# Kernel tuning notes

Hardware: AMD Instinct MI355X
Metric: run time of the kernel (lower is better)

## Reference

```python
import jax, jax.numpy as jnp
import numpy as np

B, T, C = 2, 2048, 2048
H, HD = 16, 128          # n_head, head_dim
D_C, D_C1, D_ROPE = 512, 512, 64
D_NOPE = HD - D_ROPE     # 64
M = 4                    # move_slots
EPS = 1.1920929e-07      # torch fp32 rms_norm default eps


def _rope(x, cos, sin):
    # x: (B,T,h,D), cos/sin: (B,T,D//2) -> broadcast over head axis
    c = cos[:, :, None, :]
    s = sin[:, :, None, :]
    x1, x2 = jnp.split(x, 2, axis=-1)
    return jnp.concatenate([x1 * c + x2 * s, -x1 * s + x2 * c], axis=-1)


def _rmsnorm(x):
    return x * jax.lax.rsqrt(jnp.mean(x * x, axis=-1, keepdims=True) + EPS)


def setup_inputs() -> dict:
    key = jax.random.key(0)
    ks = jax.random.split(key, 8)
    # realistic decoupled-RoPE angles over d_rope//2 frequencies
    inv_freq = 1.0 / (10000.0 ** (np.arange(0, D_ROPE, 2) / D_ROPE))  # (32,)
    ang = np.arange(T)[:, None] * inv_freq[None, :]                   # (T,32)
    cos = jnp.broadcast_to(jnp.cos(ang)[None].astype(jnp.float32), (B, T, D_ROPE // 2))
    sin = jnp.broadcast_to(jnp.sin(ang)[None].astype(jnp.float32), (B, T, D_ROPE // 2))
    return {
        "x": jax.random.normal(ks[0], (B, T, C), jnp.float32),
        "ve": jax.random.normal(ks[1], (B, T, M * H * HD), jnp.float32),
        "cos": cos,
        "sin": sin,
        "w_down": jax.random.normal(ks[2], (C, D_C + D_C1 + D_ROPE), jnp.float32) * 0.02,
        "w_ukv": jax.random.normal(ks[3], (D_C, H * (D_NOPE + HD)), jnp.float32) * 0.02,
        "w_uq": jax.random.normal(ks[4], (D_C1, H * HD), jnp.float32) * 0.02,
        "w_gate": jax.random.normal(ks[5], (C, H * (M + 1)), jnp.float32) * 0.02,
        "w_proj": jax.random.normal(ks[6], (H * HD, C), jnp.float32) * 0.02,
        "window_size": 2048,
    }


def reference(x, ve, cos, sin, w_down, w_ukv, w_uq, w_gate, w_proj, window_size):
    # fused down projection, split into kv-latent / q-latent / rope part
    down = x @ w_down                                          # (B,T,1088)
    c_kv, c_q, k_rope_raw = jnp.split(down, [D_C, D_C + D_C1], axis=-1)

    kv = (c_kv @ w_ukv).reshape(B, T, H, D_NOPE + HD)
    k_nope, v = jnp.split(kv, [D_NOPE], axis=-1)               # (B,T,H,64), (B,T,H,128)

    k_rope = _rope(k_rope_raw.reshape(B, T, 1, D_ROPE), cos, sin)  # (B,T,1,64)

    # MoVE gating: per-head gate on v plus mixture over M value-embedding slots
    ve5 = ve.reshape(B, T, M, H, HD)
    gates = 2.0 * jax.nn.sigmoid(x @ w_gate).reshape(B, T, H, M + 1)
    v = gates[..., 0:1] * v + jnp.einsum('bthm,btmhd->bthd', gates[..., 1:], ve5)

    q = (c_q @ w_uq).reshape(B, T, H, HD)
    q_nope, q_rope = jnp.split(q, [D_NOPE], axis=-1)
    q_rope = _rope(q_rope, cos, sin)

    k = jnp.concatenate([k_nope, jnp.broadcast_to(k_rope, (B, T, H, D_ROPE))], axis=-1)
    q = jnp.concatenate([q_nope, q_rope], axis=-1)
    q, k = _rmsnorm(q), _rmsnorm(k)

    # sliding-window causal attention (flash_attn semantics: j<=i and i-j<=window)
    scale = 1.0 / float(np.sqrt(HD))
    scores = jnp.einsum('bthd,bshd->bhts', q, k) * scale       # (B,H,T,T)
    i = jnp.arange(T)[:, None]
    j = jnp.arange(T)[None, :]
    mask = (j <= i) & ((i - j) <= window_size)
    scores = jnp.where(mask, scores, -jnp.inf)
    attn = jax.nn.softmax(scores, axis=-1)
    y = jnp.einsum('bhts,bshd->bthd', attn, v)                 # (B,T,H,HD)

    return y.reshape(B, T, H * HD) @ w_proj                    # (B,T,C)
```

## Files before the change

### kernel.cpp

```cpp
#include <hip/hip_runtime.h>

typedef unsigned short u16;
typedef __bf16 bfv8 __attribute__((ext_vector_type(8)));
typedef float f32x4 __attribute__((ext_vector_type(4)));
typedef u16 u16x8 __attribute__((ext_vector_type(8)));

#define B_      2
#define T_      2048
#define C_      2048
#define H_      16
#define HD_     128
#define NT_     (B_ * T_)
#define DOWN_N  1088
#define DCAT    1168
#define DCATP   1280
#define KV_N    3072
#define Q_N     2048
#define EPS_    1.1920929e-07f
#define CEXP    0.12751879524580262f

__device__ __forceinline__ float b2f(u16 u) {
    union { unsigned u; float f; } c; c.u = ((unsigned)u) << 16; return c.f;
}
__device__ __forceinline__ u16 f2b(float f) {
    union { float f; unsigned u; } c; c.f = f;
    return (u16)((c.u + 0x7FFFu + ((c.u >> 16) & 1u)) >> 16);
}
__device__ __forceinline__ float dynload(const void* p, size_t i, int bf) {
    if (bf) return b2f(((const u16*)p)[i]);
    return ((const float*)p)[i];
}

__device__ __forceinline__ void gload16(const u16* g, u16* l) {
    __builtin_amdgcn_global_load_lds(
        (const __attribute__((address_space(1))) void*)g,
        (__attribute__((address_space(3))) void*)l,
        16, 0, 0);
}

__global__ void detect_kernel(const unsigned* __restrict__ x, int* __restrict__ flag) {
    __shared__ int cnt;
    if (threadIdx.x == 0) cnt = 0;
    __syncthreads();
    int c = 0;
    for (int i = threadIdx.x; i < 4096; i += 256) {
        const unsigned w = x[i];
        const unsigned e = (w >> 7) & 0xFF;
        if (e >= 105 && e <= 140) ++c;
    }
    atomicAdd(&cnt, c);
    __syncthreads();
    if (threadIdx.x == 0) flag[0] = (cnt > 2300) ? 1 : 0;
}

__global__ __launch_bounds__(256) void cast_kernel(
    const void* __restrict__ in, u16* __restrict__ out, int n, const int* __restrict__ flagp)
{
    const int fl = flagp[0];
    const int i0 = (blockIdx.x * 256 + threadIdx.x) * 8;
    if (i0 + 8 > n) return;
    u16x8 o;
    #pragma unroll
    for (int i = 0; i < 8; ++i) o[i] = f2b(dynload(in, (size_t)i0 + i, fl));
    *(u16x8*)(out + i0) = o;
}

__global__ __launch_bounds__(256) void tcast_kernel(
    const void* __restrict__ in, u16* __restrict__ out, int K, int N, int Ntot,
    const int* __restrict__ flagp)
{
    const int fl = flagp[0];
    __shared__ float sf[32][33];
    const int n0 = blockIdx.x * 32, k0 = blockIdx.y * 32;
    const int tx = threadIdx.x & 31, ty = threadIdx.x >> 5;
    const int cr = (n0 + tx < N) ? (n0 + tx) : (N - 1);
    #pragma unroll
    for (int i = 0; i < 4; ++i)
        sf[ty + 8 * i][tx] = dynload(in, (size_t)(k0 + ty + 8 * i) * N + cr, fl);
    __syncthreads();
    #pragma unroll
    for (int i = 0; i < 4; ++i) {
        const int n = n0 + ty + 8 * i;
        if (n < Ntot) out[(size_t)n * K + k0 + tx] = (n < N) ? f2b(sf[tx][ty + 8 * i]) : (u16)0;
    }
}

__device__ __forceinline__ void stc(u16* p, float v)  { *p = f2b(v); }
__device__ __forceinline__ void stc(float* p, float v){ *p = v; }

template <typename TC>
__global__ __launch_bounds__(256) void mfma_gemm(
    const u16* __restrict__ A, int lda,
    const u16* __restrict__ BT, int ldb,
    TC* __restrict__ Cm, int ldc,
    int M, int N, int K)
{
    __shared__ u16 As[128 * 32];
    __shared__ u16 Bs[128 * 32];
    const int tid = threadIdx.x;
    const int m0 = blockIdx.y * 128, n0 = blockIdx.x * 128;
    const int w = tid >> 6, l = tid & 63;
    const int wm = (w >> 1) * 64, wn = (w & 1) * 64;
    const int lr = l & 15, lq = l >> 4;

    f32x4 acc[4][4];
    #pragma unroll
    for (int i = 0; i < 4; ++i)
        #pragma unroll
        for (int j = 0; j < 4; ++j) acc[i][j] = (f32x4){0.f, 0.f, 0.f, 0.f};

    const int srow = w * 32 + (l >> 2);
    const int scol = (l & 3) * 8;
    const u16* ag = A  + (size_t)(m0 + srow) * lda + scol;
    const u16* bg = BT + (size_t)(n0 + srow) * ldb + scol;
    u16* as0 = &As[(w * 32) * 32];
    u16* as1 = &As[(w * 32 + 16) * 32];
    u16* bs0 = &Bs[(w * 32) * 32];
    u16* bs1 = &Bs[(w * 32 + 16) * 32];

    for (int k0 = 0; k0 < K; k0 += 32) {
        gload16(ag + k0,            as0);
        gload16(ag + 16 * lda + k0, as1);
        gload16(bg + k0,            bs0);
        gload16(bg + 16 * ldb + k0, bs1);
        __syncthreads();
        bfv8 af[4], bf[4];
        #pragma unroll
        for (int mi = 0; mi < 4; ++mi) af[mi] = *(const bfv8*)&As[(wm + mi * 16 + lr) * 32 + lq * 8];
        #pragma unroll
        for (int ni = 0; ni < 4; ++ni) bf[ni] = *(const bfv8*)&Bs[(wn + ni * 16 + lr) * 32 + lq * 8];
        #pragma unroll
        for (int mi = 0; mi < 4; ++mi)
            #pragma unroll
            for (int ni = 0; ni < 4; ++ni)
                acc[mi][ni] = __builtin_amdgcn_mfma_f32_16x16x32_bf16(af[mi], bf[ni], acc[mi][ni], 0, 0, 0);
        __syncthreads();
    }

    #pragma unroll
    for (int mi = 0; mi < 4; ++mi) {
        #pragma unroll
        for (int ni = 0; ni < 4; ++ni) {
            const int col = n0 + wn + ni * 16 + lr;
            if (col < N) {
                #pragma unroll
                for (int r = 0; r < 4; ++r) {
                    const int row = m0 + wm + mi * 16 + lq * 4 + r;
                    stc(&Cm[(size_t)row * ldc + col], acc[mi][ni][r]);
                }
            }
        }
    }
}

__global__ __launch_bounds__(256) void assemble_kernel(
    const u16* __restrict__ down,
    const u16* __restrict__ qraw,
    const u16* __restrict__ kv,
    const void* __restrict__ ve,
    const void* __restrict__ cosg,
    const void* __restrict__ sing,
    u16* __restrict__ qo, u16* __restrict__ ko, u16* __restrict__ vo,
    const int* __restrict__ flagp)
{
    const int fl = flagp[0];
    const int bt = blockIdx.x;
    const int tid = threadIdx.x;
    __shared__ float cs[32], sn[32], kr[64];
    if (tid < 32) {
        cs[tid] = dynload(cosg, (size_t)bt * 32 + tid, fl);
        sn[tid] = dynload(sing, (size_t)bt * 32 + tid, fl);
    }
    __syncthreads();
    if (tid < 64) {
        const u16* rp = down + (size_t)bt * DCAT + 1024;
        const int d = tid;
        if (d < 32) kr[d] = b2f(rp[d]) * cs[d] + b2f(rp[d + 32]) * sn[d];
        else { const int r = d - 32; kr[d] = -b2f(rp[d - 32]) * sn[r] + b2f(rp[d]) * cs[r]; }
    }
    __syncthreads();

    const int h = tid >> 4;
    const int lane = tid & 15;
    const int d0 = lane * 8;

    const u16* qr = qraw + (size_t)bt * Q_N + h * HD_;
    float vq[8];
    float ss = 0.f;
    #pragma unroll
    for (int i = 0; i < 8; ++i) {
        const int d = d0 + i;
        float xv = b2f(qr[d]);
        if (d >= 64) {
            if (d < 96) { const int r = d - 64; xv = xv * cs[r] + b2f(qr[d + 32]) * sn[r]; }
            else        { const int r = d - 96; xv = -b2f(qr[d - 32]) * sn[r] + xv * cs[r]; }
        }
        vq[i] = xv; ss += xv * xv;
    }
    #pragma unroll
    for (int off = 1; off < 16; off <<= 1) ss += __shfl_xor(ss, off);
    float rms = rsqrtf(ss * (1.f / 128.f) + EPS_);
    u16* qop = qo + (size_t)bt * Q_N + h * HD_ + d0;
    #pragma unroll
    for (int i = 0; i < 8; ++i) qop[i] = f2b(vq[i] * rms);

    const u16* kvp = kv + (size_t)bt * KV_N + h * 192;
    float vk[8];
    ss = 0.f;
    #pragma unroll
    for (int i = 0; i < 8; ++i) {
        const int d = d0 + i;
        const float xv = (d < 64) ? b2f(kvp[d]) : kr[d - 64];
        vk[i] = xv; ss += xv * xv;
    }
    #pragma unroll
    for (int off = 1; off < 16; off <<= 1) ss += __shfl_xor(ss, off);
    rms = rsqrtf(ss * (1.f / 128.f) + EPS_);
    u16* kop = ko + (size_t)bt * Q_N + h * HD_ + d0;
    #pragma unroll
    for (int i = 0; i < 8; ++i) kop[i] = f2b(vk[i] * rms);

    float g[5];
    #pragma unroll
    for (int j = 0; j < 5; ++j) {
        const float logit = b2f(down[(size_t)bt * DCAT + 1088 + h * 5 + j]);
        g[j] = 2.f / (1.f + expf(-logit));
    }
    const u16* vp = kvp + 64;
    const size_t vebase = (size_t)bt * 8192 + h * HD_;
    u16* vop = vo + (size_t)bt * Q_N + h * HD_ + d0;
    #pragma unroll
    for (int i = 0; i < 8; ++i) {
        const int d = d0 + i;
        float val = g[0] * b2f(vp[d]);
        #pragma unroll
        for (int m = 0; m < 4; ++m) val += g[1 + m] * dynload(ve, vebase + m * 2048 + d, fl);
        vop[i] = f2b(val);
    }
}

__global__ __launch_bounds__(256) void vtrans_kernel(
    const u16* __restrict__ vn, u16* __restrict__ vt)
{
    __shared__ u16 s[64][72];
    const int t0 = blockIdx.x * 64;
    const int d0 = blockIdx.y * 64;
    const int bh = blockIdx.z;
    const int tid = threadIdx.x;
    {
        const int tt = tid >> 2, seg = tid & 3;
        const u16* p = vn + ((size_t)((bh >> 4) * T_) + t0 + tt) * 2048 + (bh & 15) * 128 + d0 + seg * 16;
        u16x8 v0 = *(const u16x8*)(p);
        u16x8 v1 = *(const u16x8*)(p + 8);
        *(u16x8*)&s[tt][seg * 16]     = v0;
        *(u16x8*)&s[tt][seg * 16 + 8] = v1;
    }
    __syncthreads();
    {
        const int dd = tid >> 2, tseg = tid & 3;
        u16* q = vt + ((size_t)(bh * 128) + d0 + dd) * T_ + t0 + tseg * 16;
        #pragma unroll
        for (int g = 0; g < 2; ++g) {
            u16x8 o;
            #pragma unroll
            for (int i = 0; i < 8; ++i) o[i] = s[tseg * 16 + g * 8 + i][dd];
            *(u16x8*)(q + g * 8) = o;
        }
    }
}

__global__ __launch_bounds__(512) void attn_mfma(
    const u16* __restrict__ qn, const u16* __restrict__ kn,
    const u16* __restrict__ vt, u16* __restrict__ yb,
    const int* __restrict__ wptr)
{
    __shared__ u16 Ks[64][136];
    __shared__ u16 VTs[128][72];
    __shared__ u16 Ps[8][16][72];

    const int flat = (int)(blockIdx.x + (blockIdx.y << 4) + (blockIdx.z << 8));
    const int b  = flat & 1;
    const int h  = ((flat >> 1) & 7) | ((flat >> 5) & 8);
    const int q4 = (flat >> 4) & 15;
    const int mb = ((flat ^ (flat >> 8)) & 1) ? (q4 ^ 15) : q4;
    const int m0 = mb * 128;
    const int W = wptr[0];
    const int tid = threadIdx.x;
    const int w = tid >> 6, l = tid & 63;
    const int lr = l & 15, lq = l >> 4;
    const int qr0 = m0 + w * 16;

    bfv8 qf[4];
    {
        const u16* qp = qn + ((size_t)(b * T_) + qr0 + lr) * 2048 + h * 128 + lq * 8;
        #pragma unroll
        for (int kk = 0; kk < 4; ++kk) qf[kk] = *(const bfv8*)(qp + kk * 32);
    }

    f32x4 oacc[8];
    #pragma unroll
    for (int i = 0; i < 8; ++i) oacc[i] = (f32x4){0.f, 0.f, 0.f, 0.f};
    float m_r[4] = {-1e30f, -1e30f, -1e30f, -1e30f};
    float l_r[4] = {0.f, 0.f, 0.f, 0.f};

    const int kkey = tid >> 3, kseg = tid & 7;
    const int vd = tid >> 2, vh = tid & 3;

    int ns = m0 - W; if (ns < 0) ns = 0; ns &= ~63;
    const int ne = m0 + 64;

    const u16* kbase = kn + ((size_t)(b * T_) + kkey) * 2048 + h * 128 + kseg * 16;
    const u16* vbase = vt + ((size_t)(b * H_ + h) * 128 + vd) * T_ + vh * 16;

    u16x8 pk0, pk1, pv0, pv1;
    {
        const u16* kp = kbase + (size_t)ns * 2048;
        const u16* vp = vbase + ns;
        pk0 = *(const u16x8*)(kp);
        pk1 = *(const u16x8*)(kp + 8);
        pv0 = *(const u16x8*)(vp);
        pv1 = *(const u16x8*)(vp + 8);
    }

    for (int n0 = ns; n0 <= ne; n0 += 64) {
        *(u16x8*)&Ks[kkey][kseg * 16]     = pk0;
        *(u16x8*)&Ks[kkey][kseg * 16 + 8] = pk1;
        *(u16x8*)&VTs[vd][vh * 16]        = pv0;
        *(u16x8*)&VTs[vd][vh * 16 + 8]    = pv1;
        __syncthreads();

        if (n0 < ne) {
            const u16* kp = kbase + (size_t)(n0 + 64) * 2048;
            const u16* vp = vbase + (n0 + 64);
            pk0 = *(const u16x8*)(kp);
            pk1 = *(const u16x8*)(kp + 8);
            pv0 = *(const u16x8*)(vp);
            pv1 = *(const u16x8*)(vp + 8);
        }

        const bool active = (n0 <= qr0 + 15) && (n0 + 63 >= qr0 - W);
        if (active) {
            f32x4 s[4];
            #pragma unroll
            for (int f = 0; f < 4; ++f) {
                s[f] = (f32x4){0.f, 0.f, 0.f, 0.f};
                #pragma unroll
                for (int kk = 0; kk < 4; ++kk) {
                    bfv8 kf = *(const bfv8*)&Ks[f * 16 + lr][kk * 32 + lq * 8];
                    s[f] = __builtin_amdgcn_mfma_f32_16x16x32_bf16(qf[kk], kf, s[f], 0, 0, 0);
                }
            }

            if ((n0 + 63 > qr0) || (qr0 + 15 - n0 > W)) {
                #pragma unroll
                for (int f = 0; f < 4; ++f) {
                    const int si = n0 + f * 16 + lr;
                    #pragma unroll
                    for (int r = 0; r < 4; ++r) {
                        const int ti = qr0 + lq * 4 + r;
                        if (si > ti || ti - si > W) s[f][r] = -1e30f;
                    }
                }
            }

            float al_r[4];
            #pragma unroll
            for (int r = 0; r < 4; ++r) {
                float mx = fmaxf(fmaxf(s[0][r], s[1][r]), fmaxf(s[2][r], s[3][r]));
                mx = fmaxf(mx, __shfl_xor(mx, 1));
                mx = fmaxf(mx, __shfl_xor(mx, 2));
                mx = fmaxf(mx, __shfl_xor(mx, 4));
                mx = fmaxf(mx, __shfl_xor(mx, 8));
                const float mnew = fmaxf(m_r[r], mx);
                al_r[r] = exp2f((m_r[r] - mnew) * CEXP);
                float ps = 0.f;
                #pragma unroll
                for (int f = 0; f < 4; ++f) {
                    const float sv = s[f][r];
                    const float pv = (sv <= -0.9e30f) ? 0.f : exp2f((sv - mnew) * CEXP);
                    s[f][r] = pv; ps += pv;
                }
                ps += __shfl_xor(ps, 1);
                ps += __shfl_xor(ps, 2);
                ps += __shfl_xor(ps, 4);
                ps += __shfl_xor(ps, 8);
                l_r[r] = l_r[r] * al_r[r] + ps;
                m_r[r] = mnew;
            }
            #pragma unroll
            for (int od = 0; od < 8; ++od)
                #pragma unroll
                for (int r = 0; r < 4; ++r) oacc[od][r] *= al_r[r];

            #pragma unroll
            for (int f = 0; f < 4; ++f)
                #pragma unroll
                for (int r = 0; r < 4; ++r)
                    Ps[w][lq * 4 + r][f * 16 + lr] = f2b(s[f][r]);

            #pragma unroll
            for (int kk2 = 0; kk2 < 2; ++kk2) {
                bfv8 pf = *(const bfv8*)&Ps[w][lr][kk2 * 32 + lq * 8];
                #pragma unroll
                for (int od = 0; od < 8; ++od) {
                    bfv8 vf = *(const bfv8*)&VTs[od * 16 + lr][kk2 * 32 + lq * 8];
                    oacc[od] = __builtin_amdgcn_mfma_f32_16x16x32_bf16(pf, vf, oacc[od], 0, 0, 0);
                }
            }
        }
        __syncthreads();
    }

    float inv[4];
    #pragma unroll
    for (int r = 0; r < 4; ++r) inv[r] = 1.f / l_r[r];
    #pragma unroll
    for (int od = 0; od < 8; ++od)
        #pragma unroll
        for (int r = 0; r < 4; ++r) {
            const size_t idx = ((size_t)(b * T_) + qr0 + lq * 4 + r) * 2048 + h * 128 + od * 16 + lr;
            yb[idx] = f2b(oacc[od][r] * inv[r]);
        }
}

extern "C" void kernel_launch(void* const* d_in, const int* in_sizes, int n_in,
                              void* d_out, int out_size, void* d_ws, size_t ws_size,
                              hipStream_t stream)
{
    const void* x      = d_in[0];
    const void* ve     = d_in[1];
    const void* cosg   = d_in[2];
    const void* sing   = d_in[3];
    const void* w_down = d_in[4];
    const void* w_ukv  = d_in[5];
    const void* w_uq   = d_in[6];
    const void* w_gate = d_in[7];
    const void* w_proj = d_in[8];
    const int*  wsz    = (const int*)d_in[9];
    float* out = (float*)d_out;

    char* p = (char*)d_ws;
    u16* xbf    = (u16*)p; p += (size_t)NT_ * C_ * 2;
    u16* wcatT  = (u16*)p; p += (size_t)DCATP * C_ * 2;
    u16* wukvT  = (u16*)p; p += (size_t)KV_N * 512 * 2;
    u16* wuqT   = (u16*)p; p += (size_t)Q_N * 512 * 2;
    u16* wpT    = (u16*)p; p += (size_t)C_ * C_ * 2;
    u16* downb  = (u16*)p; p += (size_t)NT_ * DCAT * 2;
    u16* kvb    = (u16*)p; p += (size_t)NT_ * KV_N * 2;
    u16* qraw   = (u16*)p; p += (size_t)NT_ * Q_N * 2;
    u16* kn     = (u16*)p; p += (size_t)NT_ * Q_N * 2;
    u16* vn     = (u16*)p; p += (size_t)NT_ * Q_N * 2;
    int* flag   = (int*)p; p += 256;
    u16* qn  = xbf;
    u16* vtb = qraw;
    u16* ybf = vn;

    dim3 blk(256);
    detect_kernel<<<1, blk, 0, stream>>>((const unsigned*)x, flag);
    cast_kernel<<<dim3(NT_ * C_ / (256 * 8)), blk, 0, stream>>>(x, xbf, NT_ * C_, flag);
    tcast_kernel<<<dim3(DOWN_N / 32, C_ / 32), blk, 0, stream>>>(w_down, wcatT, C_, DOWN_N, DOWN_N, flag);
    tcast_kernel<<<dim3((DCATP - DOWN_N) / 32, C_ / 32), blk, 0, stream>>>(
        w_gate, wcatT + (size_t)DOWN_N * C_, C_, 80, DCATP - DOWN_N, flag);
    tcast_kernel<<<dim3(KV_N / 32, 512 / 32), blk, 0, stream>>>(w_ukv, wukvT, 512, KV_N, KV_N, flag);
    tcast_kernel<<<dim3(Q_N / 32, 512 / 32), blk, 0, stream>>>(w_uq, wuqT, 512, Q_N, Q_N, flag);
    tcast_kernel<<<dim3(C_ / 32, C_ / 32), blk, 0, stream>>>(w_proj, wpT, C_, C_, C_, flag);

    mfma_gemm<u16><<<dim3(DCATP / 128, NT_ / 128), blk, 0, stream>>>(
        xbf, C_, wcatT, C_, downb, DCAT, NT_, DCAT, C_);
    mfma_gemm<u16><<<dim3(KV_N / 128, NT_ / 128), blk, 0, stream>>>(
        downb, DCAT, wukvT, 512, kvb, KV_N, NT_, KV_N, 512);
    mfma_gemm<u16><<<dim3(Q_N / 128, NT_ / 128), blk, 0, stream>>>(
        downb + 512, DCAT, wuqT, 512, qraw, Q_N, NT_, Q_N, 512);
    assemble_kernel<<<dim3(NT_), blk, 0, stream>>>(
        downb, qraw, kvb, ve, cosg, sing, qn, kn, vn, flag);
    vtrans_kernel<<<dim3(T_ / 64, 2, B_ * H_), blk, 0, stream>>>(vn, vtb);
    attn_mfma<<<dim3(T_ / 128, H_, B_), dim3(512), 0, stream>>>(qn, kn, vtb, ybf, wsz);
    mfma_gemm<float><<<dim3(Q_N / 128, NT_ / 128), blk, 0, stream>>>(
        ybf, Q_N, wpT, C_, out, C_, NT_, C_, Q_N);
}
```

Before: 677.3 us.

## Use fixed-shift softmax with MFMA row sums and two query tiles per wave

Drops the online-softmax running max and rescaling. Scores are exponentiated against a fixed shift, which is valid because q and k are RMS-normalised, so each score's magnitude is bounded by sqrt(head_dim). The row sums come from an extra MFMA against a ones column appended to the V tile, which removes the shuffle reductions. Each wave now handles 32 query rows instead of 16, reusing each K fragment twice, and the block shrinks to 256 threads with wider per-thread loads. The cost is more registers per thread and fewer waves per block, plus a reliance on the score bound holding.

```diff
diff --git a/kernel.cpp b/kernel.cpp
--- a/kernel.cpp
+++ b/kernel.cpp
@@ -18,6 +18,7 @@
 #define Q_N     2048
 #define EPS_    1.1920929e-07f
 #define CEXP    0.12751879524580262f
+#define SMAXS   16.6f
 
 __device__ __forceinline__ float b2f(u16 u) {
     union { unsigned u; float f; } c; c.u = ((unsigned)u) << 16; return c.f;
@@ -269,14 +270,14 @@
     }
 }
 
-__global__ __launch_bounds__(512) void attn_mfma(
+__global__ __launch_bounds__(256) void attn_mfma(
     const u16* __restrict__ qn, const u16* __restrict__ kn,
     const u16* __restrict__ vt, u16* __restrict__ yb,
     const int* __restrict__ wptr)
 {
     __shared__ u16 Ks[64][136];
-    __shared__ u16 VTs[128][72];
-    __shared__ u16 Ps[8][16][72];
+    __shared__ u16 VTs[144][72];
+    __shared__ u16 Ps[4][32][72];
 
     const int flat = (int)(blockIdx.x + (blockIdx.y << 4) + (blockIdx.z << 8));
     const int b  = flat & 1;
@@ -288,139 +289,149 @@
     const int tid = threadIdx.x;
     const int w = tid >> 6, l = tid & 63;
     const int lr = l & 15, lq = l >> 4;
-    const int qr0 = m0 + w * 16;
-
-    bfv8 qf[4];
+    const int qr0 = m0 + w * 32;
+
+    bfv8 qf[2][4];
+    #pragma unroll
+    for (int mi = 0; mi < 2; ++mi) {
+        const u16* qp = qn + ((size_t)(b * T_) + qr0 + mi * 16 + lr) * 2048 + h * 128 + lq * 8;
+        #pragma unroll
+        for (int kk = 0; kk < 4; ++kk) qf[mi][kk] = *(const bfv8*)(qp + kk * 32);
+    }
+
+    f32x4 oacc[2][8];
+    f32x4 lacc[2];
+    #pragma unroll
+    for (int mi = 0; mi < 2; ++mi) {
+        lacc[mi] = (f32x4){0.f, 0.f, 0.f, 0.f};
+        #pragma unroll
+        for (int od = 0; od < 8; ++od) oacc[mi][od] = (f32x4){0.f, 0.f, 0.f, 0.f};
+    }
+
     {
-        const u16* qp = qn + ((size_t)(b * T_) + qr0 + lr) * 2048 + h * 128 + lq * 8;
-        #pragma unroll
-        for (int kk = 0; kk < 4; ++kk) qf[kk] = *(const bfv8*)(qp + kk * 32);
-    }
-
-    f32x4 oacc[8];
-    #pragma unroll
-    for (int i = 0; i < 8; ++i) oacc[i] = (f32x4){0.f, 0.f, 0.f, 0.f};
-    float m_r[4] = {-1e30f, -1e30f, -1e30f, -1e30f};
-    float l_r[4] = {0.f, 0.f, 0.f, 0.f};
-
-    const int kkey = tid >> 3, kseg = tid & 7;
-    const int vd = tid >> 2, vh = tid & 3;
+        const int rr = 128 + (tid >> 4), cc = (tid & 15) * 4;
+        const u16 v = (tid >> 4) == 0 ? (u16)0x3F80 : (u16)0;
+        VTs[rr][cc] = v; VTs[rr][cc + 1] = v; VTs[rr][cc + 2] = v; VTs[rr][cc + 3] = v;
+    }
+
+    const int kkey = tid >> 2, kq = tid & 3;
+    const int vd = tid >> 1, vh2 = tid & 1;
 
     int ns = m0 - W; if (ns < 0) ns = 0; ns &= ~63;
     const int ne = m0 + 64;
 
-    const u16* kbase = kn + ((size_t)(b * T_) + kkey) * 2048 + h * 128 + kseg * 16;
-    const u16* vbase = vt + ((size_t)(b * H_ + h) * 128 + vd) * T_ + vh * 16;
-
-    u16x8 pk0, pk1, pv0, pv1;
+    const u16* kbase = kn + ((size_t)(b * T_) + kkey) * 2048 + h * 128 + kq * 32;
+    const u16* vbase = vt + ((size_t)(b * H_ + h) * 128 + vd) * T_ + vh2 * 32;
+
+    u16x8 pk[4], pv[4];
     {
         const u16* kp = kbase + (size_t)ns * 2048;
         const u16* vp = vbase + ns;
-        pk0 = *(const u16x8*)(kp);
-        pk1 = *(const u16x8*)(kp + 8);
-        pv0 = *(const u16x8*)(vp);
-        pv1 = *(const u16x8*)(vp + 8);
+        #pragma unroll
+        for (int s = 0; s < 4; ++s) pk[s] = *(const u16x8*)(kp + s * 8);
+        #pragma unroll
+        for (int s = 0; s < 4; ++s) pv[s] = *(const u16x8*)(vp + s * 8);
     }
 
     for (int n0 = ns; n0 <= ne; n0 += 64) {
-        *(u16x8*)&Ks[kkey][kseg * 16]     = pk0;
-        *(u16x8*)&Ks[kkey][kseg * 16 + 8] = pk1;
-        *(u16x8*)&VTs[vd][vh * 16]        = pv0;
-        *(u16x8*)&VTs[vd][vh * 16 + 8]    = pv1;
+        {
+            u16* kd = &Ks[kkey][kq * 32];
+            #pragma unroll
+            for (int s = 0; s < 4; ++s) *(u16x8*)(kd + s * 8) = pk[s];
+            u16* vdst = &VTs[vd][vh2 * 32];
+            #pragma unroll
+            for (int s = 0; s < 4; ++s) *(u16x8*)(vdst + s * 8) = pv[s];
+        }
         __syncthreads();
 
         if (n0 < ne) {
             const u16* kp = kbase + (size_t)(n0 + 64) * 2048;
             const u16* vp = vbase + (n0 + 64);
-            pk0 = *(const u16x8*)(kp);
-            pk1 = *(const u16x8*)(kp + 8);
-            pv0 = *(const u16x8*)(vp);
-            pv1 = *(const u16x8*)(vp + 8);
-        }
-
-        const bool active = (n0 <= qr0 + 15) && (n0 + 63 >= qr0 - W);
+            #pragma unroll
+            for (int s = 0; s < 4; ++s) pk[s] = *(const u16x8*)(kp + s * 8);
+            #pragma unroll
+            for (int s = 0; s < 4; ++s) pv[s] = *(const u16x8*)(vp + s * 8);
+        }
+
+        const bool active = (n0 <= qr0 + 31) && (n0 + 63 >= qr0 - W);
         if (active) {
-            f32x4 s[4];
+            f32x4 s0[4], s1[4];
             #pragma unroll
             for (int f = 0; f < 4; ++f) {
-                s[f] = (f32x4){0.f, 0.f, 0.f, 0.f};
+                f32x4 a0 = (f32x4){0.f, 0.f, 0.f, 0.f};
+                f32x4 a1 = (f32x4){0.f, 0.f, 0.f, 0.f};
                 #pragma unroll
                 for (int kk = 0; kk < 4; ++kk) {
                     bfv8 kf = *(const bfv8*)&Ks[f * 16 + lr][kk * 32 + lq * 8];
-                    s[f] = __builtin_amdgcn_mfma_f32_16x16x32_bf16(qf[kk], kf, s[f], 0, 0, 0);
+                    a0 = __builtin_amdgcn_mfma_f32_16x16x32_bf16(qf[0][kk], kf, a0, 0, 0, 0);
+                    a1 = __builtin_amdgcn_mfma_f32_16x16x32_bf16(qf[1][kk], kf, a1, 0, 0, 0);
                 }
-            }
-
-            if ((n0 + 63 > qr0) || (qr0 + 15 - n0 > W)) {
+                s0[f] = a0; s1[f] = a1;
+            }
+
+            if ((n0 + 63 > qr0) || (qr0 + 31 - n0 > W)) {
                 #pragma unroll
                 for (int f = 0; f < 4; ++f) {
                     const int si = n0 + f * 16 + lr;
                     #pragma unroll
                     for (int r = 0; r < 4; ++r) {
-                        const int ti = qr0 + lq * 4 + r;
-                        if (si > ti || ti - si > W) s[f][r] = -1e30f;
+                        const int t0i = qr0 + lq * 4 + r;
+                        const int t1i = t0i + 16;
+                        if (si > t0i || t0i - si > W) s0[f][r] = -1e30f;
+                        if (si > t1i || t1i - si > W) s1[f][r] = -1e30f;
                     }
                 }
             }
 
-            float al_r[4];
-            #pragma unroll
-            for (int r = 0; r < 4; ++r) {
-                float mx = fmaxf(fmaxf(s[0][r], s[1][r]), fmaxf(s[2][r], s[3][r]));
-                mx = fmaxf(mx, __shfl_xor(mx, 1));
-                mx = fmaxf(mx, __shfl_xor(mx, 2));
-                mx = fmaxf(mx, __shfl_xor(mx, 4));
-                mx = fmaxf(mx, __shfl_xor(mx, 8));
-                const float mnew = fmaxf(m_r[r], mx);
-                al_r[r] = exp2f((m_r[r] - mnew) * CEXP);
-                float ps = 0.f;
-                #pragma unroll
-                for (int f = 0; f < 4; ++f) {
-                    const float sv = s[f][r];
-                    const float pv = (sv <= -0.9e30f) ? 0.f : exp2f((sv - mnew) * CEXP);
-                    s[f][r] = pv; ps += pv;
-                }
-                ps += __shfl_xor(ps, 1);
-                ps += __shfl_xor(ps, 2);
-                ps += __shfl_xor(ps, 4);
-                ps += __shfl_xor(ps, 8);
-                l_r[r] = l_r[r] * al_r[r] + ps;
-                m_r[r] = mnew;
-            }
-            #pragma unroll
-            for (int od = 0; od < 8; ++od)
-                #pragma unroll
-                for (int r = 0; r < 4; ++r) oacc[od][r] *= al_r[r];
-
             #pragma unroll
             for (int f = 0; f < 4; ++f)
                 #pragma unroll
-                for (int r = 0; r < 4; ++r)
-                    Ps[w][lq * 4 + r][f * 16 + lr] = f2b(s[f][r]);
-
+                for (int r = 0; r < 4; ++r) {
+                    const float p0 = exp2f(s0[f][r] * CEXP - SMAXS);
+                    const float p1 = exp2f(s1[f][r] * CEXP - SMAXS);
+                    Ps[w][lq * 4 + r][f * 16 + lr]      = f2b(p0);
+                    Ps[w][16 + lq * 4 + r][f * 16 + lr] = f2b(p1);
+                }
+
+            bfv8 pf0[2], pf1[2];
             #pragma unroll
             for (int kk2 = 0; kk2 < 2; ++kk2) {
-                bfv8 pf = *(const bfv8*)&Ps[w][lr][kk2 * 32 + lq * 8];
+                pf0[kk2] = *(const bfv8*)&Ps[w][lr][kk2 * 32 + lq * 8];
+                pf1[kk2] = *(const bfv8*)&Ps[w][16 + lr][kk2 * 32 + lq * 8];
+            }
+            #pragma unroll
+            for (int kk2 = 0; kk2 < 2; ++kk2) {
                 #pragma unroll
                 for (int od = 0; od < 8; ++od) {
                     bfv8 vf = *(const bfv8*)&VTs[od * 16 + lr][kk2 * 32 + lq * 8];
-                    oacc[od] = __builtin_amdgcn_mfma_f32_16x16x32_bf16(pf, vf, oacc[od], 0, 0, 0);
+                    oacc[0][od] = __builtin_amdgcn_mfma_f32_16x16x32_bf16(pf0[kk2], vf, oacc[0][od], 0, 0, 0);
+                    oacc[1][od] = __builtin_amdgcn_mfma_f32_16x16x32_bf16(pf1[kk2], vf, oacc[1][od], 0, 0, 0);
                 }
+                bfv8 vf1 = *(const bfv8*)&VTs[128 + lr][kk2 * 32 + lq * 8];
+                lacc[0] = __builtin_amdgcn_mfma_f32_16x16x32_bf16(pf0[kk2], vf1, lacc[0], 0, 0, 0);
+                lacc[1] = __builtin_amdgcn_mfma_f32_16x16x32_bf16(pf1[kk2], vf1, lacc[1], 0, 0, 0);
             }
         }
         __syncthreads();
     }
 
-    float inv[4];
-    #pragma unroll
-    for (int r = 0; r < 4; ++r) inv[r] = 1.f / l_r[r];
-    #pragma unroll
-    for (int od = 0; od < 8; ++od)
+    #pragma unroll
+    for (int mi = 0; mi < 2; ++mi) {
+        float linv[4];
         #pragma unroll
         for (int r = 0; r < 4; ++r) {
-            const size_t idx = ((size_t)(b * T_) + qr0 + lq * 4 + r) * 2048 + h * 128 + od * 16 + lr;
-            yb[idx] = f2b(oacc[od][r] * inv[r]);
-        }
+            const float lv = __shfl(lacc[mi][r], l & 48);
+            linv[r] = 1.f / lv;
+        }
+        #pragma unroll
+        for (int od = 0; od < 8; ++od)
+            #pragma unroll
+            for (int r = 0; r < 4; ++r) {
+                const size_t idx = ((size_t)(b * T_) + qr0 + mi * 16 + lq * 4 + r) * 2048
+                                 + h * 128 + od * 16 + lr;
+                yb[idx] = f2b(oacc[mi][od][r] * linv[r]);
+            }
+    }
 }
 
 extern "C" void kernel_launch(void* const* d_in, const int* in_sizes, int n_in,
@@ -474,7 +485,7 @@
     assemble_kernel<<<dim3(NT_), blk, 0, stream>>>(
         downb, qraw, kvb, ve, cosg, sing, qn, kn, vn, flag);
     vtrans_kernel<<<dim3(T_ / 64, 2, B_ * H_), blk, 0, stream>>>(vn, vtb);
-    attn_mfma<<<dim3(T_ / 128, H_, B_), dim3(512), 0, stream>>>(qn, kn, vtb, ybf, wsz);
+    attn_mfma<<<dim3(T_ / 128, H_, B_), dim3(256), 0, stream>>>(qn, kn, vtb, ybf, wsz);
     mfma_gemm<float><<<dim3(Q_N / 128, NT_ / 128), blk, 0, stream>>>(
         ybf, Q_N, wpT, C_, out, C_, NT_, C_, Q_N);
 }
```

Measured after the change: 659.6 us. 2.6% less time.
